# Optimization experiments

Measured on AMD Instinct MI355X. Metric: run time of the kernel, lower is better.

The kernel has to match this reference:

```python
import jax, jax.numpy as jnp
import numpy as np

H, DH = 16, 64          # num_heads, dim_head
DIM = 1024              # dim_ltn
EPS = 1e-5


def setup_inputs() -> dict:
    key = jax.random.key(0)
    ks = jax.random.split(key, 8)
    b, n_txt, t, m = 2, 2048, 4, 256
    text = jax.random.normal(ks[0], (b, n_txt, DIM), dtype=jnp.float32)
    image = jax.random.normal(ks[1], (b, t, m, DIM), dtype=jnp.float32)
    locations = jax.random.randint(ks[2], (b, n_txt), 0, 2)  # 0/1 media markers
    s = DIM ** -0.5
    Wq = jax.random.normal(ks[3], (DIM, H * DH), dtype=jnp.float32) * s
    Wkv = jax.random.normal(ks[4], (DIM, 2 * H * DH), dtype=jnp.float32) * s
    Wo = jax.random.normal(ks[5], (H * DH, DIM), dtype=jnp.float32) * s
    ln_gamma = jnp.ones((DIM,), dtype=jnp.float32)
    ln_beta = jnp.zeros((DIM,), dtype=jnp.float32)
    return {"text": text, "image": image, "locations": locations,
            "Wq": Wq, "Wkv": Wkv, "Wo": Wo,
            "ln_gamma": ln_gamma, "ln_beta": ln_beta}


def reference(text, image, locations, Wq, Wkv, Wo, ln_gamma, ln_beta):
    scale = DH ** -0.5
    b, t, m, d = image.shape
    # LayerNorm(text)
    mu = text.mean(-1, keepdims=True)
    var = ((text - mu) ** 2).mean(-1, keepdims=True)
    tn = (text - mu) / jnp.sqrt(var + EPS) * ln_gamma + ln_beta
    img = image.reshape(b, t * m, d)             # b (t m) d
    q = tn @ Wq                                  # b n (h dh)
    k, v = jnp.split(img @ Wkv, 2, axis=-1)      # each b tm (h dh)
    split_heads = lambda x: x.reshape(x.shape[0], x.shape[1], H, DH).transpose(0, 2, 1, 3)
    q, k, v = split_heads(q), split_heads(k), split_heads(v)
    attn = jnp.einsum('bhid,bhjd->bhij', q, k) * scale   # b h n (t m)
    txt_time = jnp.cumsum(locations, axis=-1)            # b n : media index per text token
    viz_time = jnp.repeat(jnp.arange(1, t + 1), m)       # (t m)
    # only_attend_to_immediate -> equality mask
    mask = txt_time[:, None, :, None] == viz_time[None, None, None, :]
    neg = -jnp.finfo(attn.dtype).max
    attn = jnp.where(mask, attn, neg)
    attn = jax.nn.softmax(attn, axis=-1)
    # zero attention for text tokens before any media (txt_time == 0)
    attn = jnp.where((txt_time == 0)[:, None, :, None], 0.0, attn)
    out = jnp.einsum('bhij,bhjd->bhid', attn, v)
    out = out.transpose(0, 2, 1, 3).reshape(b, -1, H * DH)
    return out @ Wo
```

## Files before the change

### kernel.cpp

```cpp
#include <hip/hip_runtime.h>

#define BATCH 2
#define NTXT  2048
#define TMED  4
#define MMED  256
#define TM    (TMED * MMED)
#define DIM   1024
#define NH    16
#define DHD   64
#define KVW   2048
#define RMAX  256
#define RT    32

typedef _Float16 f16x8 __attribute__((ext_vector_type(8)));
typedef float    f32x4 __attribute__((ext_vector_type(4)));

__global__ __launch_bounds__(1024) void k1_scan_cvt_tr(
    const int* __restrict__ loc, const float* __restrict__ image,
    const float* __restrict__ Wkv, int* __restrict__ tt, int* __restrict__ seg,
    float* __restrict__ ipart, _Float16* __restrict__ img16,
    _Float16* __restrict__ WkvT, float* __restrict__ zbase) {
  __shared__ float tile[64][65];
  __shared__ int wtot[16];
  __shared__ int wmin[2][16];
  const int idx = blockIdx.x;
  const int tid = threadIdx.x;
  if (idx < BATCH) {
    const int b = idx;
    const int lane = tid & 63, w = tid >> 6;
    const int e0 = tid * 2;
    const int a0 = loc[b * NTXT + e0], a1 = loc[b * NTXT + e0 + 1];
    const int p = a0 + a1;
    int incl = p;
#pragma unroll
    for (int off = 1; off < 64; off <<= 1) {
      const int t2 = __shfl_up(incl, off, 64);
      if (lane >= off) incl += t2;
    }
    if (lane == 63) wtot[w] = incl;
    __syncthreads();
    if (tid < 16) {
      const int v = wtot[tid];
      int inc2 = v;
#pragma unroll
      for (int off = 1; off < 16; off <<= 1) {
        const int t3 = __shfl_up(inc2, off, 64);
        if (tid >= off) inc2 += t3;
      }
      wtot[tid] = inc2 - v;
    }
    __syncthreads();
    const int base = wtot[w] + (incl - p);
    const int t0v = base + a0, t1v = t0v + a1;
    tt[b * NTXT + e0]     = t0v;
    tt[b * NTXT + e0 + 1] = t1v;
    {
      const int c1 = (t1v >= 1) ? ((t0v >= 1) ? e0 : e0 + 1) : NTXT;
      const int c5 = (t1v >= 5) ? ((t0v >= 5) ? e0 : e0 + 1) : NTXT;
      const unsigned long long b1 = __ballot(t1v >= 1);
      const unsigned long long b5 = __ballot(t1v >= 5);
      int m1 = NTXT, m5 = NTXT;
      if (b1) m1 = __shfl(c1, __ffsll(b1) - 1, 64);
      if (b5) m5 = __shfl(c5, __ffsll(b5) - 1, 64);
      if (lane == 0) { wmin[0][w] = m1; wmin[1][w] = m5; }
    }
    __syncthreads();
    if (tid == 0) {
      int s = NTXT, e = NTXT;
#pragma unroll
      for (int i = 0; i < 16; i++) {
        s = min(s, wmin[0][i]);
        e = min(e, wmin[1][i]);
      }
      seg[b * 2]     = s;
      seg[b * 2 + 1] = e - s;
    }
  } else if (idx < BATCH + 256) {
    const int j = idx - BATCH;
    const int b = j >> 7, rt = j & 127;
    const size_t base = (size_t)(b * TM + rt * 8) * DIM + tid;
    const float* p = image + base;
    _Float16* q = img16 + base;
    float s = 0.f;
#pragma unroll
    for (int r = 0; r < 8; r++) {
      const float v = p[(size_t)r * DIM];
      s += v;
      q[(size_t)r * DIM] = (_Float16)v;
    }
    ipart[(size_t)(b * 128 + rt) * DIM + tid] = s;
  } else if (idx < BATCH + 256 + 512) {
    const int j2 = idx - BATCH - 256;
    const int k0 = (j2 & 15) * 64, n0 = (j2 >> 4) * 64;
    const int r = tid >> 4, c4 = (tid & 15) * 4;
    const float4 v = *reinterpret_cast<const float4*>(
        Wkv + (size_t)(k0 + r) * KVW + n0 + c4);
    tile[r][c4 + 0] = v.x; tile[r][c4 + 1] = v.y;
    tile[r][c4 + 2] = v.z; tile[r][c4 + 3] = v.w;
    __syncthreads();
    if (tid < 512) {
      const int n = tid >> 3, kc = (tid & 7) * 8;
      f16x8 h;
#pragma unroll
      for (int u = 0; u < 8; u++) h[u] = (_Float16)tile[kc + u][n];
      *reinterpret_cast<f16x8*>(WkvT + (size_t)(n0 + n) * DIM + k0 + kc) = h;
    }
  } else {
    const int j = idx - (BATCH + 256 + 512);
    float4* z = reinterpret_cast<float4*>(zbase);
    const float4 zv = {0.f, 0.f, 0.f, 0.f};
    for (int i = j * 1024 + tid; i < 132096; i += 16 * 1024) z[i] = zv;
  }
}

__global__ __launch_bounds__(256) void k2_prep(
    const float* __restrict__ Wkv, const float* __restrict__ text,
    const float* __restrict__ gamma, const float* __restrict__ beta,
    const int* __restrict__ seg, const float* __restrict__ ipart,
    float* __restrict__ tn, float* __restrict__ vbar,
    float* __restrict__ out) {
  __shared__ float red[256];
  const int idx = blockIdx.x;
  const int tid = threadIdx.x;
  if (idx < 64) {
    const int b = idx >> 5, rt = idx & 31;
    const int i0 = seg[b * 2];
    const int cnt = min(seg[b * 2 + 1], RMAX);
    for (int r = rt; r < cnt; r += RT) {
      const float* xrow = text + (size_t)(b * NTXT + i0 + r) * DIM;
      float x[4];
      float s = 0.f;
#pragma unroll
      for (int u = 0; u < 4; u++) { x[u] = xrow[tid + 256 * u]; s += x[u]; }
      red[tid] = s; __syncthreads();
      for (int st = 128; st > 0; st >>= 1) {
        if (tid < st) red[tid] += red[tid + st];
        __syncthreads();
      }
      const float mu = red[0] * (1.0f / DIM); __syncthreads();
      float vs = 0.f;
#pragma unroll
      for (int u = 0; u < 4; u++) { float d = x[u] - mu; vs += d * d; }
      red[tid] = vs; __syncthreads();
      for (int st = 128; st > 0; st >>= 1) {
        if (tid < st) red[tid] += red[tid + st];
        __syncthreads();
      }
      const float rstd = rsqrtf(red[0] * (1.0f / DIM) + 1e-5f); __syncthreads();
      float* trow = tn + (size_t)(b * RMAX + r) * DIM;
#pragma unroll
      for (int u = 0; u < 4; u++) {
        const int c = tid + 256 * u;
        trow[c] = (x[u] - mu) * rstd * gamma[c] + beta[c];
      }
      __syncthreads();
    }
  } else if (idx < 128) {
    const int j = idx - 64;
    const int b = j >> 5, et = (j >> 3) & 3, cc = j & 7;
    const int e = et * 256 + tid;
    const int c0 = cc * 128;
    if (tid < 128) {
      float s = 0.f;
      for (int p = 0; p < 128; p++)
        s += ipart[(size_t)(b * 128 + p) * DIM + c0 + tid];
      red[tid] = s * (1.0f / (float)TM);
    }
    __syncthreads();
    float s = 0.f;
    for (int c = 0; c < 128; c++)
      s += red[c] * Wkv[(size_t)(c0 + c) * KVW + DIM + e];
    atomicAdd(&vbar[b * DIM + e], s);
  } else {
    const int b = idx - 128;
    const int i0 = seg[b * 2];
    const int cnt = min(seg[b * 2 + 1], RMAX);
    for (int r = 0; r < cnt; r++) {
      float* orow = out + (size_t)(b * NTXT + i0 + r) * DIM;
      for (int c = tid; c < DIM; c += 256) orow[c] = 0.f;
    }
  }
}

__global__ __launch_bounds__(512) void k3_gemm_qproj_obar(
    const _Float16* __restrict__ img16, const _Float16* __restrict__ WkvT,
    const float* __restrict__ Wq, const float* __restrict__ Wo,
    const float* __restrict__ tn, const float* __restrict__ vbar,
    const int* __restrict__ seg, _Float16* __restrict__ kv16,
    float* __restrict__ qbuf, float* __restrict__ obar) {
  __shared__ __align__(16) char smem[32768];
  const int idx = blockIdx.x;
  const int tid = threadIdx.x;
  if (idx < 256) {
    _Float16* As = (_Float16*)smem;
    _Float16* Bs = As + 128 * 64;
    const int lane = tid & 63, wid = tid >> 6;
    const int wm = wid & 3, wn = wid >> 2;
    const int row0 = (idx >> 4) * 128, col0 = (idx & 15) * 128;
    const int srow = tid >> 3, skc = (tid & 7) * 8;
    const int frow = lane & 15, fq = lane >> 4;
    const int swk = skc ^ ((srow & 7) << 3);
    f32x4 acc[2][4] = {};
    f16x8 a0v = *reinterpret_cast<const f16x8*>(
        img16 + (size_t)(row0 + srow) * DIM + skc);
    f16x8 a1v = *reinterpret_cast<const f16x8*>(
        img16 + (size_t)(row0 + srow + 64) * DIM + skc);
    f16x8 b0v = *reinterpret_cast<const f16x8*>(
        WkvT + (size_t)(col0 + srow) * DIM + skc);
    f16x8 b1v = *reinterpret_cast<const f16x8*>(
        WkvT + (size_t)(col0 + srow + 64) * DIM + skc);
    for (int k0 = 0; k0 < DIM; k0 += 64) {
      __syncthreads();
      *reinterpret_cast<f16x8*>(As + srow * 64 + swk)        = a0v;
      *reinterpret_cast<f16x8*>(As + (srow + 64) * 64 + swk) = a1v;
      *reinterpret_cast<f16x8*>(Bs + srow * 64 + swk)        = b0v;
      *reinterpret_cast<f16x8*>(Bs + (srow + 64) * 64 + swk) = b1v;
      __syncthreads();
      if (k0 + 64 < DIM) {
        a0v = *reinterpret_cast<const f16x8*>(
            img16 + (size_t)(row0 + srow) * DIM + k0 + 64 + skc);
        a1v = *reinterpret_cast<const f16x8*>(
            img16 + (size_t)(row0 + srow + 64) * DIM + k0 + 64 + skc);
        b0v = *reinterpret_cast<const f16x8*>(
            WkvT + (size_t)(col0 + srow) * DIM + k0 + 64 + skc);
        b1v = *reinterpret_cast<const f16x8*>(
            WkvT + (size_t)(col0 + srow + 64) * DIM + k0 + 64 + skc);
      }
      f16x8 af[2][2], bf[2][4];
#pragma unroll
      for (int kk = 0; kk < 2; kk++) {
#pragma unroll
        for (int mt = 0; mt < 2; mt++) {
          const int r = wm * 32 + mt * 16 + frow;
          af[kk][mt] = *reinterpret_cast<const f16x8*>(
              As + r * 64 + ((kk * 32 + fq * 8) ^ ((r & 7) << 3)));
        }
#pragma unroll
        for (int nt = 0; nt < 4; nt++) {
          const int c = wn * 64 + nt * 16 + frow;
          bf[kk][nt] = *reinterpret_cast<const f16x8*>(
              Bs + c * 64 + ((kk * 32 + fq * 8) ^ ((c & 7) << 3)));
        }
      }
#pragma unroll
      for (int kk = 0; kk < 2; kk++)
#pragma unroll
        for (int mt = 0; mt < 2; mt++)
#pragma unroll
          for (int nt = 0; nt < 4; nt++)
            acc[mt][nt] = __builtin_amdgcn_mfma_f32_16x16x32_f16(
                af[kk][mt], bf[kk][nt], acc[mt][nt], 0, 0, 0);
    }
#pragma unroll
    for (int mt = 0; mt < 2; mt++)
#pragma unroll
      for (int nt = 0; nt < 4; nt++) {
        const int col = col0 + wn * 64 + nt * 16 + frow;
#pragma unroll
        for (int r = 0; r < 4; r++) {
          const int row = row0 + wm * 32 + mt * 16 + fq * 4 + r;
          kv16[(size_t)row * KVW + col] = (_Float16)acc[mt][nt][r];
        }
      }
  } else if (idx < 320) {
    float* tn_s = (float*)smem;
    const int j = idx - 256;
    const int b = j >> 5, nt = (j >> 2) & 7, cc = j & 3;
    const int n0 = nt * 128, c0 = cc * 256;
    const int n = tid & 127, cs = tid >> 7;
    const int cnt = min(seg[b * 2 + 1], RMAX);
    for (int r0 = 0; r0 < cnt; r0 += 8) {
      const int rows = min(8, cnt - r0);
      for (int i = tid; i < 8 * 256; i += 512) {
        const int r = i >> 8, c = i & 255;
        tn_s[i] = (r < rows) ? tn[(size_t)(b * RMAX + r0 + r) * DIM + c0 + c]
                             : 0.f;
      }
      __syncthreads();
      float acc[8] = {};
      for (int ci = 0; ci < 64; ci++) {
        const int c = cs * 64 + ci;
        const float w = Wq[(size_t)(c0 + c) * DIM + n0 + n];
#pragma unroll
        for (int rr = 0; rr < 8; rr++) acc[rr] += tn_s[rr * 256 + c] * w;
      }
      for (int rr = 0; rr < rows; rr++)
        atomicAdd(&qbuf[(size_t)(b * RMAX + r0 + rr) * DIM + n0 + n], acc[rr]);
      __syncthreads();
    }
  } else {
    float* vb_s = (float*)smem;
    const int j = idx - 320;
    const int b = j >> 4, et = (j >> 3) & 1, cc = j & 7;
    const int e = et * 512 + tid;
    const int c0 = cc * 128;
    if (tid < 128) vb_s[tid] = vbar[b * DIM + c0 + tid];
    __syncthreads();
    float s = 0.f;
    for (int c = 0; c < 128; c++)
      s += vb_s[c] * Wo[(size_t)(c0 + c) * DIM + e];
    atomicAdd(&obar[b * DIM + e], s);
  }
}

__global__ __launch_bounds__(256) void k4_fill_attn(
    const float* __restrict__ text, const _Float16* __restrict__ kv16,
    const float* __restrict__ Wq, const float* __restrict__ Wo,
    const float* __restrict__ gamma, const float* __restrict__ beta,
    const int* __restrict__ tt, const int* __restrict__ seg,
    const float* __restrict__ obar, const float* __restrict__ qbuf,
    float* __restrict__ out) {
  __shared__ float red[256];
  __shared__ float pbuf[256];
  const int idx = blockIdx.x;
  const int tid = threadIdx.x;
  if (idx < BATCH * NTXT) {
    const int b = idx >> 11;
    const int i = idx & (NTXT - 1);
    const int t = tt[b * NTXT + i];
    float* orow = out + (size_t)(b * NTXT + i) * DIM;
    if (t == 0) {
      for (int c = tid; c < DIM; c += 256) orow[c] = 0.f;
      return;
    }
    if (t > TMED) {
      const float* ob = obar + b * DIM;
      for (int c = tid; c < DIM; c += 256) orow[c] = ob[c];
      return;
    }
    if (i - seg[b * 2] < RMAX) return;
    __shared__ float tns[DIM];
    __shared__ float qrow[DIM];
    __shared__ float oaccs[DIM];
    const float* xrow = text + (size_t)(b * NTXT + i) * DIM;
    float x[4];
    float s = 0.f;
#pragma unroll
    for (int u = 0; u < 4; u++) { x[u] = xrow[tid + 256 * u]; s += x[u]; }
    red[tid] = s; __syncthreads();
    for (int st = 128; st > 0; st >>= 1) {
      if (tid < st) red[tid] += red[tid + st];
      __syncthreads();
    }
    const float mu = red[0] * (1.0f / DIM); __syncthreads();
    float vs = 0.f;
#pragma unroll
    for (int u = 0; u < 4; u++) { float d = x[u] - mu; vs += d * d; }
    red[tid] = vs; __syncthreads();
    for (int st = 128; st > 0; st >>= 1) {
      if (tid < st) red[tid] += red[tid + st];
      __syncthreads();
    }
    const float rstd = rsqrtf(red[0] * (1.0f / DIM) + 1e-5f); __syncthreads();
#pragma unroll
    for (int u = 0; u < 4; u++) {
      const int c = tid + 256 * u;
      tns[c] = (x[u] - mu) * rstd * gamma[c] + beta[c];
    }
    __syncthreads();
    {
      float qa[4] = {0.f, 0.f, 0.f, 0.f};
      for (int c = 0; c < DIM; c++) {
        const float tv = tns[c];
        const float* w = Wq + (size_t)c * DIM + tid;
#pragma unroll
        for (int u = 0; u < 4; u++) qa[u] += tv * w[256 * u];
      }
#pragma unroll
      for (int u = 0; u < 4; u++) qrow[tid + 256 * u] = qa[u];
    }
    __syncthreads();
    const size_t kvrow0 = (size_t)(b * TM + (t - 1) * MMED) * KVW;
    const int d0 = tid & 63, g = tid >> 6;
    for (int h = 0; h < NH; h++) {
      const _Float16* krow = kv16 + kvrow0 + (size_t)tid * KVW + h * DHD;
      float sc = 0.f;
#pragma unroll
      for (int d = 0; d < DHD; d++) sc += qrow[h * DHD + d] * (float)krow[d];
      sc *= 0.125f;
      red[tid] = sc; __syncthreads();
      for (int st = 128; st > 0; st >>= 1) {
        if (tid < st) red[tid] = fmaxf(red[tid], red[tid + st]);
        __syncthreads();
      }
      const float mx = red[0]; __syncthreads();
      const float e = __expf(sc - mx);
      red[tid] = e; __syncthreads();
      for (int st = 128; st > 0; st >>= 1) {
        if (tid < st) red[tid] += red[tid + st];
        __syncthreads();
      }
      const float inv = 1.0f / red[0]; __syncthreads();
      pbuf[tid] = e * inv; __syncthreads();
      const _Float16* vbase = kv16 + kvrow0 + (size_t)(g * 64) * KVW + DIM + h * DHD + d0;
      float a = 0.f;
#pragma unroll 8
      for (int jj = 0; jj < 64; jj++) a += pbuf[g * 64 + jj] * (float)vbase[(size_t)jj * KVW];
      red[tid] = a; __syncthreads();
      if (tid < 64)
        oaccs[h * DHD + tid] = red[tid] + red[64 + tid] + red[128 + tid] + red[192 + tid];
      __syncthreads();
    }
    float oa[4] = {0.f, 0.f, 0.f, 0.f};
    for (int c = 0; c < DIM; c++) {
      const float ov = oaccs[c];
      const float* w = Wo + (size_t)c * DIM + tid;
#pragma unroll
      for (int u = 0; u < 4; u++) oa[u] += ov * w[256 * u];
    }
#pragma unroll
    for (int u = 0; u < 4; u++) orow[tid + 256 * u] = oa[u];
  } else {
    __shared__ float qs[DHD];
    __shared__ float osl[DHD];
    const int j = idx - BATCH * NTXT;
    const int h = j & 15, rt = (j >> 4) & 31, b = j >> 9;
    const int i0 = seg[b * 2];
    const int cnt = min(seg[b * 2 + 1], RMAX);
    const int d0 = tid & 63, g = tid >> 6;
    for (int r = rt; r < cnt; r += RT) {
      const int i = i0 + r;
      const int t = tt[b * NTXT + i];
      if (tid < 64) qs[tid] = qbuf[(size_t)(b * RMAX + r) * DIM + h * DHD + tid];
      __syncthreads();
      const size_t kvrow0 = (size_t)(b * TM + (t - 1) * MMED) * KVW;
      const _Float16* krow = kv16 + kvrow0 + (size_t)tid * KVW + h * DHD;
      float sc = 0.f;
#pragma unroll
      for (int d = 0; d < DHD; d += 8) {
        const f16x8 kk = *reinterpret_cast<const f16x8*>(krow + d);
#pragma unroll
        for (int u = 0; u < 8; u++) sc += qs[d + u] * (float)kk[u];
      }
      sc *= 0.125f;
      red[tid] = sc; __syncthreads();
      for (int st = 128; st > 0; st >>= 1) {
        if (tid < st) red[tid] = fmaxf(red[tid], red[tid + st]);
        __syncthreads();
      }
      const float mx = red[0]; __syncthreads();
      const float e = __expf(sc - mx);
      red[tid] = e; __syncthreads();
      for (int st = 128; st > 0; st >>= 1) {
        if (tid < st) red[tid] += red[tid + st];
        __syncthreads();
      }
      const float inv = 1.0f / red[0]; __syncthreads();
      pbuf[tid] = e * inv; __syncthreads();
      const _Float16* vbase = kv16 + kvrow0 + (size_t)(g * 64) * KVW + DIM + h * DHD + d0;
      float a = 0.f;
#pragma unroll 8
      for (int jj = 0; jj < 64; jj++) a += pbuf[g * 64 + jj] * (float)vbase[(size_t)jj * KVW];
      red[tid] = a; __syncthreads();
      if (tid < 64)
        osl[tid] = red[tid] + red[64 + tid] + red[128 + tid] + red[192 + tid];
      __syncthreads();
      float* orow = out + (size_t)(b * NTXT + i) * DIM;
#pragma unroll
      for (int u = 0; u < 4; u++) {
        const int c = tid + 256 * u;
        const float* w = Wo + (size_t)(h * DHD) * DIM + c;
        float s2 = 0.f;
#pragma unroll 8
        for (int d = 0; d < DHD; d++) s2 += osl[d] * w[(size_t)d * DIM];
        atomicAdd(&orow[c], s2);
      }
      __syncthreads();
    }
  }
}

extern "C" void kernel_launch(void* const* d_in, const int* in_sizes, int n_in,
                              void* d_out, int out_size, void* d_ws, size_t ws_size,
                              hipStream_t stream) {
  const float* text  = (const float*)d_in[0];
  const float* image = (const float*)d_in[1];
  const int*   loc   = (const int*)d_in[2];
  const float* Wq    = (const float*)d_in[3];
  const float* Wkv   = (const float*)d_in[4];
  const float* Wo    = (const float*)d_in[5];
  const float* gamma = (const float*)d_in[6];
  const float* beta  = (const float*)d_in[7];
  float* out = (float*)d_out;

  _Float16* kv16  = (_Float16*)d_ws;
  _Float16* WkvT  = kv16 + (size_t)BATCH * TM * KVW;
  _Float16* img16 = WkvT + (size_t)KVW * DIM;
  float*    tn    = (float*)(img16 + (size_t)BATCH * TM * DIM);
  float*    qbuf  = tn + (size_t)BATCH * RMAX * DIM;
  float*    vbar  = qbuf + (size_t)BATCH * RMAX * DIM;
  float*    obar  = vbar + BATCH * DIM;
  int*      tt    = (int*)(obar + BATCH * DIM);
  int*      seg   = tt + BATCH * NTXT;
  float*    ipart = (float*)(seg + 8);

  k1_scan_cvt_tr<<<BATCH + 256 + 512 + 16, 1024, 0, stream>>>(
      loc, image, Wkv, tt, seg, ipart, img16, WkvT, qbuf);
  k2_prep<<<130, 256, 0, stream>>>(Wkv, text, gamma, beta, seg, ipart,
                                   tn, vbar, out);
  k3_gemm_qproj_obar<<<352, 512, 0, stream>>>(img16, WkvT, Wq, Wo, tn, vbar,
                                              seg, kv16, qbuf, obar);
  k4_fill_attn<<<BATCH * NTXT + NH * RT * BATCH, 256, 0, stream>>>(
      text, kv16, Wq, Wo, gamma, beta, tt, seg, obar, qbuf, out);
}
```

Measured before the change: 152.8 us.

## Fuse image fp16 conversion into KV GEMM and drop img16 buffer

k1 no longer writes an fp16 copy of the image. The KV projection GEMM now reads fp32 image directly and converts it to fp16 while staging into shared memory. The K tile shrinks from 64 to 32 and the register prefetch and LDS swizzle are removed. Block indices are remapped for locality, and the zero and obar row fills use float4 stores. This removes a full write and reread of the image in fp16, at the cost of more global bytes read per A tile, no prefetch overlap, and possible LDS bank conflicts.

```diff
diff --git a/kernel.cpp b/kernel.cpp
--- a/kernel.cpp
+++ b/kernel.cpp
@@ -18,8 +18,8 @@
 __global__ __launch_bounds__(1024) void k1_scan_cvt_tr(
     const int* __restrict__ loc, const float* __restrict__ image,
     const float* __restrict__ Wkv, int* __restrict__ tt, int* __restrict__ seg,
-    float* __restrict__ ipart, _Float16* __restrict__ img16,
-    _Float16* __restrict__ WkvT, float* __restrict__ zbase) {
+    float* __restrict__ ipart, _Float16* __restrict__ WkvT,
+    float* __restrict__ zbase) {
   __shared__ float tile[64][65];
   __shared__ int wtot[16];
   __shared__ int wmin[2][16];
@@ -80,14 +80,9 @@
     const int b = j >> 7, rt = j & 127;
     const size_t base = (size_t)(b * TM + rt * 8) * DIM + tid;
     const float* p = image + base;
-    _Float16* q = img16 + base;
     float s = 0.f;
 #pragma unroll
-    for (int r = 0; r < 8; r++) {
-      const float v = p[(size_t)r * DIM];
-      s += v;
-      q[(size_t)r * DIM] = (_Float16)v;
-    }
+    for (int r = 0; r < 8; r++) s += p[(size_t)r * DIM];
     ipart[(size_t)(b * 128 + rt) * DIM + tid] = s;
   } else if (idx < BATCH + 256 + 512) {
     const int j2 = idx - BATCH - 256;
@@ -183,73 +178,54 @@
 }
 
 __global__ __launch_bounds__(512) void k3_gemm_qproj_obar(
-    const _Float16* __restrict__ img16, const _Float16* __restrict__ WkvT,
+    const float* __restrict__ image, const _Float16* __restrict__ WkvT,
     const float* __restrict__ Wq, const float* __restrict__ Wo,
     const float* __restrict__ tn, const float* __restrict__ vbar,
     const int* __restrict__ seg, _Float16* __restrict__ kv16,
     float* __restrict__ qbuf, float* __restrict__ obar) {
-  __shared__ __align__(16) char smem[32768];
+  __shared__ __align__(16) char smem[16384];
   const int idx = blockIdx.x;
   const int tid = threadIdx.x;
   if (idx < 256) {
     _Float16* As = (_Float16*)smem;
-    _Float16* Bs = As + 128 * 64;
+    _Float16* Bs = As + 128 * 32;
+    const int swz = (idx & 7) * 32 + (idx >> 3);
     const int lane = tid & 63, wid = tid >> 6;
     const int wm = wid & 3, wn = wid >> 2;
-    const int row0 = (idx >> 4) * 128, col0 = (idx & 15) * 128;
-    const int srow = tid >> 3, skc = (tid & 7) * 8;
+    const int row0 = (swz >> 4) * 128, col0 = (swz & 15) * 128;
+    const int srow = tid >> 2, skc = (tid & 3) * 8;
     const int frow = lane & 15, fq = lane >> 4;
-    const int swk = skc ^ ((srow & 7) << 3);
+    const float*    aptr = image + (size_t)(row0 + srow) * DIM + skc;
+    const _Float16* bptr = WkvT + (size_t)(col0 + srow) * DIM + skc;
     f32x4 acc[2][4] = {};
-    f16x8 a0v = *reinterpret_cast<const f16x8*>(
-        img16 + (size_t)(row0 + srow) * DIM + skc);
-    f16x8 a1v = *reinterpret_cast<const f16x8*>(
-        img16 + (size_t)(row0 + srow + 64) * DIM + skc);
-    f16x8 b0v = *reinterpret_cast<const f16x8*>(
-        WkvT + (size_t)(col0 + srow) * DIM + skc);
-    f16x8 b1v = *reinterpret_cast<const f16x8*>(
-        WkvT + (size_t)(col0 + srow + 64) * DIM + skc);
-    for (int k0 = 0; k0 < DIM; k0 += 64) {
-      __syncthreads();
-      *reinterpret_cast<f16x8*>(As + srow * 64 + swk)        = a0v;
-      *reinterpret_cast<f16x8*>(As + (srow + 64) * 64 + swk) = a1v;
-      *reinterpret_cast<f16x8*>(Bs + srow * 64 + swk)        = b0v;
-      *reinterpret_cast<f16x8*>(Bs + (srow + 64) * 64 + swk) = b1v;
-      __syncthreads();
-      if (k0 + 64 < DIM) {
-        a0v = *reinterpret_cast<const f16x8*>(
-            img16 + (size_t)(row0 + srow) * DIM + k0 + 64 + skc);
-        a1v = *reinterpret_cast<const f16x8*>(
-            img16 + (size_t)(row0 + srow + 64) * DIM + k0 + 64 + skc);
-        b0v = *reinterpret_cast<const f16x8*>(
-            WkvT + (size_t)(col0 + srow) * DIM + k0 + 64 + skc);
-        b1v = *reinterpret_cast<const f16x8*>(
-            WkvT + (size_t)(col0 + srow + 64) * DIM + k0 + 64 + skc);
-      }
-      f16x8 af[2][2], bf[2][4];
-#pragma unroll
-      for (int kk = 0; kk < 2; kk++) {
-#pragma unroll
-        for (int mt = 0; mt < 2; mt++) {
-          const int r = wm * 32 + mt * 16 + frow;
-          af[kk][mt] = *reinterpret_cast<const f16x8*>(
-              As + r * 64 + ((kk * 32 + fq * 8) ^ ((r & 7) << 3)));
-        }
-#pragma unroll
-        for (int nt = 0; nt < 4; nt++) {
-          const int c = wn * 64 + nt * 16 + frow;
-          bf[kk][nt] = *reinterpret_cast<const f16x8*>(
-              Bs + c * 64 + ((kk * 32 + fq * 8) ^ ((c & 7) << 3)));
-        }
-      }
-#pragma unroll
-      for (int kk = 0; kk < 2; kk++)
-#pragma unroll
-        for (int mt = 0; mt < 2; mt++)
-#pragma unroll
-          for (int nt = 0; nt < 4; nt++)
-            acc[mt][nt] = __builtin_amdgcn_mfma_f32_16x16x32_f16(
-                af[kk][mt], bf[kk][nt], acc[mt][nt], 0, 0, 0);
+    for (int k0 = 0; k0 < DIM; k0 += 32) {
+      const float4 av0 = *reinterpret_cast<const float4*>(aptr + k0);
+      const float4 av1 = *reinterpret_cast<const float4*>(aptr + k0 + 4);
+      const f16x8 bv = *reinterpret_cast<const f16x8*>(bptr + k0);
+      f16x8 ah;
+      ah[0] = (_Float16)av0.x; ah[1] = (_Float16)av0.y;
+      ah[2] = (_Float16)av0.z; ah[3] = (_Float16)av0.w;
+      ah[4] = (_Float16)av1.x; ah[5] = (_Float16)av1.y;
+      ah[6] = (_Float16)av1.z; ah[7] = (_Float16)av1.w;
+      __syncthreads();
+      *reinterpret_cast<f16x8*>(As + tid * 8) = ah;
+      *reinterpret_cast<f16x8*>(Bs + tid * 8) = bv;
+      __syncthreads();
+      f16x8 af[2], bf[4];
+#pragma unroll
+      for (int mt = 0; mt < 2; mt++)
+        af[mt] = *reinterpret_cast<const f16x8*>(
+            As + (wm * 32 + mt * 16 + frow) * 32 + fq * 8);
+#pragma unroll
+      for (int nt = 0; nt < 4; nt++)
+        bf[nt] = *reinterpret_cast<const f16x8*>(
+            Bs + (wn * 64 + nt * 16 + frow) * 32 + fq * 8);
+#pragma unroll
+      for (int mt = 0; mt < 2; mt++)
+#pragma unroll
+        for (int nt = 0; nt < 4; nt++)
+          acc[mt][nt] = __builtin_amdgcn_mfma_f32_16x16x32_f16(
+              af[mt], bf[nt], acc[mt][nt], 0, 0, 0);
     }
 #pragma unroll
     for (int mt = 0; mt < 2; mt++)
@@ -320,12 +296,13 @@
     const int t = tt[b * NTXT + i];
     float* orow = out + (size_t)(b * NTXT + i) * DIM;
     if (t == 0) {
-      for (int c = tid; c < DIM; c += 256) orow[c] = 0.f;
+      const float4 zv = {0.f, 0.f, 0.f, 0.f};
+      reinterpret_cast<float4*>(orow)[tid] = zv;
       return;
     }
     if (t > TMED) {
-      const float* ob = obar + b * DIM;
-      for (int c = tid; c < DIM; c += 256) orow[c] = ob[c];
+      reinterpret_cast<float4*>(orow)[tid] =
+          reinterpret_cast<const float4*>(obar + b * DIM)[tid];
       return;
     }
     if (i - seg[b * 2] < RMAX) return;
@@ -485,8 +462,7 @@
 
   _Float16* kv16  = (_Float16*)d_ws;
   _Float16* WkvT  = kv16 + (size_t)BATCH * TM * KVW;
-  _Float16* img16 = WkvT + (size_t)KVW * DIM;
-  float*    tn    = (float*)(img16 + (size_t)BATCH * TM * DIM);
+  float*    tn    = (float*)(WkvT + (size_t)KVW * DIM);
   float*    qbuf  = tn + (size_t)BATCH * RMAX * DIM;
   float*    vbar  = qbuf + (size_t)BATCH * RMAX * DIM;
   float*    obar  = vbar + BATCH * DIM;
@@ -495,10 +471,10 @@
   float*    ipart = (float*)(seg + 8);
 
   k1_scan_cvt_tr<<<BATCH + 256 + 512 + 16, 1024, 0, stream>>>(
-      loc, image, Wkv, tt, seg, ipart, img16, WkvT, qbuf);
+      loc, image, Wkv, tt, seg, ipart, WkvT, qbuf);
   k2_prep<<<130, 256, 0, stream>>>(Wkv, text, gamma, beta, seg, ipart,
                                    tn, vbar, out);
-  k3_gemm_qproj_obar<<<352, 512, 0, stream>>>(img16, WkvT, Wq, Wo, tn, vbar,
+  k3_gemm_qproj_obar<<<352, 512, 0, stream>>>(image, WkvT, Wq, Wo, tn, vbar,
                                               seg, kv16, qbuf, obar);
   k4_fill_attn<<<BATCH * NTXT + NH * RT * BATCH, 256, 0, stream>>>(
       text, kv16, Wq, Wo, gamma, beta, tt, seg, obar, qbuf, out);
```

Measured after the change: 152.7 us. Within noise of the previous version (-0.1%).
